# Performance work log

Measured on AMD Instinct MI355X. Metric: run time of the kernel, lower is better.

The kernel has to match this reference:

```python
import jax, jax.numpy as jnp
import numpy as np

N_QUBITS = 2
Q_DEPTH = 2
B = 2_097_152


def _rot(phi, theta, omega):
    """PennyLane Rot gate: RZ(omega) @ RY(theta) @ RZ(phi), shape [2,2] complex."""
    ct = jnp.cos(theta * 0.5)
    st = jnp.sin(theta * 0.5)
    m00 = jnp.exp(-0.5j * (phi + omega)) * ct
    m01 = -jnp.exp(0.5j * (phi - omega)) * st
    m10 = jnp.exp(-0.5j * (phi - omega)) * st
    m11 = jnp.exp(0.5j * (phi + omega)) * ct
    return jnp.stack([jnp.stack([m00, m01]), jnp.stack([m10, m11])])


def _circuit(noise, q_weights):
    # AngleEmbedding (RX rotations) applied to |00>: state = RX(a0)|0> (x) RX(a1)|0>
    angles = noise.astype(jnp.float32) * jnp.pi  # original: rand * pi
    c = jnp.cos(angles * 0.5)                    # [B,2]
    s = jnp.sin(angles * 0.5)
    v0 = jnp.stack([c[:, 0] + 0j, -1j * s[:, 0]], axis=1)  # [B,2] amps of qubit 0
    v1 = jnp.stack([c[:, 1] + 0j, -1j * s[:, 1]], axis=1)  # [B,2] amps of qubit 1
    state = v0[:, :, None] * v1[:, None, :]                # [B,2,2] statevector

    # StronglyEntanglingLayers: per layer Rot on each wire, then CNOT ring (r=1)
    for l in range(Q_DEPTH):
        g0 = _rot(q_weights[l, 0, 0], q_weights[l, 0, 1], q_weights[l, 0, 2])
        g1 = _rot(q_weights[l, 1, 0], q_weights[l, 1, 1], q_weights[l, 1, 2])
        state = jnp.einsum('ij,bjk->bik', g0, state)  # gate on qubit 0
        state = jnp.einsum('ij,bkj->bki', g1, state)  # gate on qubit 1
        # CNOT(control=0, target=1): flip qubit-1 index where qubit-0 == 1
        state = jnp.stack([state[:, 0, :], state[:, 1, ::-1]], axis=1)
        # CNOT(control=1, target=0): flip qubit-0 index where qubit-1 == 1
        state = jnp.stack([state[:, :, 0], state[:, ::-1, 1]], axis=2)

    probs = jnp.abs(state) ** 2  # [B,2,2]
    z0 = probs[:, 0, :].sum(-1) - probs[:, 1, :].sum(-1)  # <Z> on wire 0
    z1 = probs[:, :, 0].sum(-1) - probs[:, :, 1].sum(-1)  # <Z> on wire 1
    return jnp.stack([z0, z1], axis=1).astype(jnp.float32)  # [B,2]


def setup_inputs() -> dict:
    key = jax.random.key(0)
    k1, k2 = jax.random.split(key)
    noise = jax.random.uniform(k1, (B, N_QUBITS), dtype=jnp.float32)
    q_weights = 0.1 * jax.random.normal(k2, (Q_DEPTH, N_QUBITS, 3), dtype=jnp.float32)
    return {"noise": noise, "q_weights": q_weights}


def reference(noise, q_weights):
    return _circuit(noise, q_weights)
```

## Files before the change

### kernel.cpp

```cpp
#include <hip/hip_runtime.h>
#include <math.h>


struct Cx { float re, im; };
__device__ inline Cx cmul(Cx a, Cx b){ return {a.re*b.re - a.im*b.im, a.re*b.im + a.im*b.re}; }
__device__ inline Cx cmadd2(Cx a, Cx x, Cx b, Cx y){
  Cx p = cmul(a,x), q = cmul(b,y);
  return { p.re + q.re, p.im + q.im };
}

__global__ void qc_prep(const float* __restrict__ w, float* __restrict__ K) {
  if (threadIdx.x != 0) return;

  Cx U[4][4];
  for (int r = 0; r < 4; ++r)
    for (int c = 0; c < 4; ++c)
      U[r][c] = { (r == c) ? 1.f : 0.f, 0.f };

  for (int l = 0; l < 2; ++l) {
    Cx g[2][2][2];
    for (int q = 0; q < 2; ++q) {
      float phi = w[l*6 + q*3 + 0];
      float th  = w[l*6 + q*3 + 1];
      float om  = w[l*6 + q*3 + 2];
      float st, ct; sincosf(0.5f*th, &st, &ct);
      float sp, cp; sincosf(0.5f*(phi+om), &sp, &cp);
      float sm, cm; sincosf(0.5f*(phi-om), &sm, &cm);
      g[q][0][0] = {  cp*ct, -sp*ct };
      g[q][0][1] = { -cm*st, -sm*st };
      g[q][1][0] = {  cm*st, -sm*st };
      g[q][1][1] = {  cp*ct,  sp*ct };
    }
    for (int c = 0; c < 4; ++c)
      for (int k = 0; k < 2; ++k) {
        Cx x0 = U[k][c], x1 = U[2+k][c];
        U[k][c]   = cmadd2(g[0][0][0], x0, g[0][0][1], x1);
        U[2+k][c] = cmadd2(g[0][1][0], x0, g[0][1][1], x1);
      }
    for (int c = 0; c < 4; ++c)
      for (int j = 0; j < 2; ++j) {
        Cx x0 = U[2*j][c], x1 = U[2*j+1][c];
        U[2*j][c]   = cmadd2(g[1][0][0], x0, g[1][0][1], x1);
        U[2*j+1][c] = cmadd2(g[1][1][0], x0, g[1][1][1], x1);
      }
    for (int c = 0; c < 4; ++c) { Cx t = U[2][c]; U[2][c] = U[3][c]; U[3][c] = t; }
    for (int c = 0; c < 4; ++c) { Cx t = U[1][c]; U[1][c] = U[3][c]; U[3][c] = t; }
  }

  for (int r = 0; r < 4; ++r) {
    Cx t;
    t = U[r][1]; U[r][1] = {  t.im, -t.re };
    t = U[r][2]; U[r][2] = {  t.im, -t.re };
    t = U[r][3]; U[r][3] = { -t.re, -t.im };
  }

  const float z0s[4] = { 1.f,  1.f, -1.f, -1.f };
  const float z1s[4] = { 1.f, -1.f,  1.f, -1.f };
  float A[2][16];
  for (int a = 0; a < 4; ++a)
    for (int b = 0; b < 4; ++b) {
      float a0 = 0.f, a1 = 0.f;
      for (int r = 0; r < 4; ++r) {
        float d = U[r][a].re*U[r][b].re + U[r][a].im*U[r][b].im;
        a0 += z0s[r]*d;
        a1 += z1s[r]*d;
      }
      A[0][a*4 + b] = a0;
      A[1][a*4 + b] = a1;
    }

  float M[2][9];
  for (int q = 0; q < 2; ++q) {
    const float* a = A[q];
    M[q][0] = a[0];
    M[q][1] = 2.f*a[1];
    M[q][2] = a[5];
    M[q][3] = 2.f*a[2];
    M[q][4] = 2.f*(a[3]+a[6]);
    M[q][5] = 2.f*a[7];
    M[q][6] = a[10];
    M[q][7] = 2.f*a[11];
    M[q][8] = a[15];
  }

  const float T[3][3] = { {0.5f, 0.5f, 0.f},
                          {0.f,  0.f,  0.5f},
                          {0.5f, -0.5f, 0.f} };
  for (int q = 0; q < 2; ++q)
    for (int c = 0; c < 3; ++c)
      for (int d = 0; d < 3; ++d) {
        float acc = 0.f;
        for (int a = 0; a < 3; ++a)
          for (int b = 0; b < 3; ++b)
            acc += T[a][c] * M[q][a*3+b] * T[b][d];
        K[q*9 + c*3 + d] = acc;
      }
}

__device__ inline float evalK(const float* __restrict__ k,
                              float C0, float S0, float C1, float S1) {
  float t0 = fmaf(k[2], S1, fmaf(k[1], C1, k[0]));
  float t1 = fmaf(k[5], S1, fmaf(k[4], C1, k[3]));
  float t2 = fmaf(k[8], S1, fmaf(k[7], C1, k[6]));
  return fmaf(S0, t2, fmaf(C0, t1, t0));
}

__global__ __launch_bounds__(256) void qc_main(const float* __restrict__ noise,
                                               const float* __restrict__ Kg,
                                               float* __restrict__ out,
                                               int nQuads) {
  float k0[9], k1[9];
  #pragma unroll
  for (int i = 0; i < 9; ++i) { k0[i] = Kg[i]; k1[i] = Kg[9 + i]; }

  const float PI = 3.14159265358979323846f;
  const float4* __restrict__ in4  = (const float4*)noise;
  float4* __restrict__ out4 = (float4*)out;

  int i = blockIdx.x * blockDim.x + threadIdx.x;
  if (i >= nQuads) return;

  float4 v = in4[i];
  float4 o;
  {
    float S0, C0, S1, C1;
    __sincosf(v.x * PI, &S0, &C0);
    __sincosf(v.y * PI, &S1, &C1);
    o.x = evalK(k0, C0, S0, C1, S1);
    o.y = evalK(k1, C0, S0, C1, S1);
  }
  {
    float S0, C0, S1, C1;
    __sincosf(v.z * PI, &S0, &C0);
    __sincosf(v.w * PI, &S1, &C1);
    o.z = evalK(k0, C0, S0, C1, S1);
    o.w = evalK(k1, C0, S0, C1, S1);
  }
  out4[i] = o;
}

extern "C" void kernel_launch(void* const* d_in, const int* in_sizes, int n_in,
                              void* d_out, int out_size, void* d_ws, size_t ws_size,
                              hipStream_t stream) {
  const float* noise = (const float*)d_in[0];
  const float* w     = (const float*)d_in[1];
  float* out         = (float*)d_out;
  float* K           = (float*)d_ws;

  qc_prep<<<1, 64, 0, stream>>>(w, K);

  int nQuads  = in_sizes[0] / 4;
  int threads = 256;
  int blocks  = (nQuads + threads - 1) / threads;
  qc_main<<<blocks, threads, 0, stream>>>(noise, K, out, nQuads);
}
```

Measured before the change: 73.60 us.

## Fuse coefficient prep into main kernel and use hardware sin/cos

Removes the separate single-thread prep kernel. Each block's first thread now computes the 18 expectation coefficients into shared memory, and the block synchronizes before evaluating. The main evaluation uses the native AMD sin/cos builtins, which take their argument in revolutions, in place of __sincosf. Block size rises to 1024. This drops one launch and its inter-kernel dependency, at the cost of redundant serial prep work in every block and a barrier stall.

```diff
diff --git a/kernel.cpp b/kernel.cpp
--- a/kernel.cpp
+++ b/kernel.cpp
@@ -9,44 +9,53 @@
   return { p.re + q.re, p.im + q.im };
 }
 
-__global__ void qc_prep(const float* __restrict__ w, float* __restrict__ K) {
-  if (threadIdx.x != 0) return;
-
+__device__ void compute_K(const float* __restrict__ w, float* __restrict__ K) {
   Cx U[4][4];
+  #pragma unroll
   for (int r = 0; r < 4; ++r)
+    #pragma unroll
     for (int c = 0; c < 4; ++c)
       U[r][c] = { (r == c) ? 1.f : 0.f, 0.f };
 
+  #pragma unroll
   for (int l = 0; l < 2; ++l) {
     Cx g[2][2][2];
+    #pragma unroll
     for (int q = 0; q < 2; ++q) {
       float phi = w[l*6 + q*3 + 0];
       float th  = w[l*6 + q*3 + 1];
       float om  = w[l*6 + q*3 + 2];
-      float st, ct; sincosf(0.5f*th, &st, &ct);
-      float sp, cp; sincosf(0.5f*(phi+om), &sp, &cp);
-      float sm, cm; sincosf(0.5f*(phi-om), &sm, &cm);
+      float st, ct; __sincosf(0.5f*th, &st, &ct);
+      float sp, cp; __sincosf(0.5f*(phi+om), &sp, &cp);
+      float sm, cm; __sincosf(0.5f*(phi-om), &sm, &cm);
       g[q][0][0] = {  cp*ct, -sp*ct };
       g[q][0][1] = { -cm*st, -sm*st };
       g[q][1][0] = {  cm*st, -sm*st };
       g[q][1][1] = {  cp*ct,  sp*ct };
     }
+    #pragma unroll
     for (int c = 0; c < 4; ++c)
+      #pragma unroll
       for (int k = 0; k < 2; ++k) {
         Cx x0 = U[k][c], x1 = U[2+k][c];
         U[k][c]   = cmadd2(g[0][0][0], x0, g[0][0][1], x1);
         U[2+k][c] = cmadd2(g[0][1][0], x0, g[0][1][1], x1);
       }
+    #pragma unroll
     for (int c = 0; c < 4; ++c)
+      #pragma unroll
       for (int j = 0; j < 2; ++j) {
         Cx x0 = U[2*j][c], x1 = U[2*j+1][c];
         U[2*j][c]   = cmadd2(g[1][0][0], x0, g[1][0][1], x1);
         U[2*j+1][c] = cmadd2(g[1][1][0], x0, g[1][1][1], x1);
       }
+    #pragma unroll
     for (int c = 0; c < 4; ++c) { Cx t = U[2][c]; U[2][c] = U[3][c]; U[3][c] = t; }
+    #pragma unroll
     for (int c = 0; c < 4; ++c) { Cx t = U[1][c]; U[1][c] = U[3][c]; U[3][c] = t; }
   }
 
+  #pragma unroll
   for (int r = 0; r < 4; ++r) {
     Cx t;
     t = U[r][1]; U[r][1] = {  t.im, -t.re };
@@ -57,9 +66,12 @@
   const float z0s[4] = { 1.f,  1.f, -1.f, -1.f };
   const float z1s[4] = { 1.f, -1.f,  1.f, -1.f };
   float A[2][16];
+  #pragma unroll
   for (int a = 0; a < 4; ++a)
+    #pragma unroll
     for (int b = 0; b < 4; ++b) {
       float a0 = 0.f, a1 = 0.f;
+      #pragma unroll
       for (int r = 0; r < 4; ++r) {
         float d = U[r][a].re*U[r][b].re + U[r][a].im*U[r][b].im;
         a0 += z0s[r]*d;
@@ -69,32 +81,34 @@
       A[1][a*4 + b] = a1;
     }
 
-  float M[2][9];
-  for (int q = 0; q < 2; ++q) {
-    const float* a = A[q];
-    M[q][0] = a[0];
-    M[q][1] = 2.f*a[1];
-    M[q][2] = a[5];
-    M[q][3] = 2.f*a[2];
-    M[q][4] = 2.f*(a[3]+a[6]);
-    M[q][5] = 2.f*a[7];
-    M[q][6] = a[10];
-    M[q][7] = 2.f*a[11];
-    M[q][8] = a[15];
-  }
-
   const float T[3][3] = { {0.5f, 0.5f, 0.f},
                           {0.f,  0.f,  0.5f},
                           {0.5f, -0.5f, 0.f} };
-  for (int q = 0; q < 2; ++q)
+  #pragma unroll
+  for (int q = 0; q < 2; ++q) {
+    const float* a = A[q];
+    float M[9];
+    M[0] = a[0];
+    M[1] = 2.f*a[1];
+    M[2] = a[5];
+    M[3] = 2.f*a[2];
+    M[4] = 2.f*(a[3]+a[6]);
+    M[5] = 2.f*a[7];
+    M[6] = a[10];
+    M[7] = 2.f*a[11];
+    M[8] = a[15];
+    float tmp[9];
+    #pragma unroll
+    for (int r = 0; r < 3; ++r)
+      #pragma unroll
+      for (int d = 0; d < 3; ++d)
+        tmp[r*3+d] = M[r*3+0]*T[0][d] + M[r*3+1]*T[1][d] + M[r*3+2]*T[2][d];
+    #pragma unroll
     for (int c = 0; c < 3; ++c)
-      for (int d = 0; d < 3; ++d) {
-        float acc = 0.f;
-        for (int a = 0; a < 3; ++a)
-          for (int b = 0; b < 3; ++b)
-            acc += T[a][c] * M[q][a*3+b] * T[b][d];
-        K[q*9 + c*3 + d] = acc;
-      }
+      #pragma unroll
+      for (int d = 0; d < 3; ++d)
+        K[q*9 + c*3 + d] = T[0][c]*tmp[0*3+d] + T[1][c]*tmp[1*3+d] + T[2][c]*tmp[2*3+d];
+  }
 }
 
 __device__ inline float evalK(const float* __restrict__ k,
@@ -105,34 +119,44 @@
   return fmaf(S0, t2, fmaf(C0, t1, t0));
 }
 
-__global__ __launch_bounds__(256) void qc_main(const float* __restrict__ noise,
-                                               const float* __restrict__ Kg,
-                                               float* __restrict__ out,
-                                               int nQuads) {
-  float k0[9], k1[9];
-  #pragma unroll
-  for (int i = 0; i < 9; ++i) { k0[i] = Kg[i]; k1[i] = Kg[9 + i]; }
+__global__ __launch_bounds__(1024) void qc_fused(const float* __restrict__ noise,
+                                                 const float* __restrict__ w,
+                                                 float* __restrict__ out,
+                                                 int nQuads) {
+  __shared__ float sK[18];
 
-  const float PI = 3.14159265358979323846f;
   const float4* __restrict__ in4  = (const float4*)noise;
   float4* __restrict__ out4 = (float4*)out;
 
   int i = blockIdx.x * blockDim.x + threadIdx.x;
-  if (i >= nQuads) return;
+  bool valid = (i < nQuads);
 
-  float4 v = in4[i];
+  float4 v = {0.f, 0.f, 0.f, 0.f};
+  if (valid) v = in4[i];
+
+  if (threadIdx.x == 0) compute_K(w, sK);
+  __syncthreads();
+
+  float k0[9], k1[9];
+  #pragma unroll
+  for (int j = 0; j < 9; ++j) { k0[j] = sK[j]; k1[j] = sK[9 + j]; }
+
+  if (!valid) return;
+
   float4 o;
   {
-    float S0, C0, S1, C1;
-    __sincosf(v.x * PI, &S0, &C0);
-    __sincosf(v.y * PI, &S1, &C1);
+    float C0 = __builtin_amdgcn_cosf(0.5f * v.x);
+    float S0 = __builtin_amdgcn_sinf(0.5f * v.x);
+    float C1 = __builtin_amdgcn_cosf(0.5f * v.y);
+    float S1 = __builtin_amdgcn_sinf(0.5f * v.y);
     o.x = evalK(k0, C0, S0, C1, S1);
     o.y = evalK(k1, C0, S0, C1, S1);
   }
   {
-    float S0, C0, S1, C1;
-    __sincosf(v.z * PI, &S0, &C0);
-    __sincosf(v.w * PI, &S1, &C1);
+    float C0 = __builtin_amdgcn_cosf(0.5f * v.z);
+    float S0 = __builtin_amdgcn_sinf(0.5f * v.z);
+    float C1 = __builtin_amdgcn_cosf(0.5f * v.w);
+    float S1 = __builtin_amdgcn_sinf(0.5f * v.w);
     o.z = evalK(k0, C0, S0, C1, S1);
     o.w = evalK(k1, C0, S0, C1, S1);
   }
@@ -145,12 +169,9 @@
   const float* noise = (const float*)d_in[0];
   const float* w     = (const float*)d_in[1];
   float* out         = (float*)d_out;
-  float* K           = (float*)d_ws;
-
-  qc_prep<<<1, 64, 0, stream>>>(w, K);
 
   int nQuads  = in_sizes[0] / 4;
-  int threads = 256;
+  int threads = 1024;
   int blocks  = (nQuads + threads - 1) / threads;
-  qc_main<<<blocks, threads, 0, stream>>>(noise, K, out, nQuads);
+  qc_fused<<<blocks, threads, 0, stream>>>(noise, w, out, nQuads);
 }
```

New measurement: 77.56 us. +5.4%, slower.
